# Performance work log

Measured on AMD Instinct MI355X. Metric: run time of the kernel, lower is better.

Reference implementation:

```python
import jax, jax.numpy as jnp
import numpy as np

D_MODEL = 1024
N_HEADS = 16
D_K = D_MODEL // N_HEADS
SCALE = float(np.sqrt(D_K))


def setup_inputs() -> dict:
    key = jax.random.key(0)
    ks = jax.random.split(key, 12)
    B, S = 2, 2048
    std = 1.0 / np.sqrt(D_MODEL)
    inp = {
        "query": jax.random.normal(ks[0], (B, S, D_MODEL), jnp.float32),
        "key": jax.random.normal(ks[1], (B, S, D_MODEL), jnp.float32),
        "value": jax.random.normal(ks[2], (B, S, D_MODEL), jnp.float32),
        "mask": jnp.ones((B, S), jnp.int32),
        "Wq": jax.random.normal(ks[3], (D_MODEL, D_MODEL), jnp.float32) * std,
        "bq": jnp.zeros((D_MODEL,), jnp.float32),
        "Wk": jax.random.normal(ks[4], (D_MODEL, D_MODEL), jnp.float32) * std,
        "bk": jnp.zeros((D_MODEL,), jnp.float32),
        "Wv": jax.random.normal(ks[5], (D_MODEL, D_MODEL), jnp.float32) * std,
        "bv": jnp.zeros((D_MODEL,), jnp.float32),
        "Wo": jax.random.normal(ks[6], (D_MODEL, D_MODEL), jnp.float32) * std,
        "bo": jnp.zeros((D_MODEL,), jnp.float32),
    }
    return inp


def reference(query, key, value, mask, Wq, bq, Wk, bk, Wv, bv, Wo, bo):
    B, S, _ = query.shape
    # projections -> [B, H, S, d_k]
    def proj(x, W, b):
        return (x @ W.T + b).reshape(B, S, N_HEADS, D_K).transpose(0, 2, 1, 3)

    Q = proj(query, Wq, bq)
    K = proj(key, Wk, bk)
    V = proj(value, Wv, bv)
    # [B, H, Sq, Sk] scores
    scores = jnp.einsum("bhqd,bhkd->bhqk", Q, K) / SCALE
    m = mask[:, None, None, :]  # broadcast over heads and query positions
    scores = jnp.where(m == 0, jnp.float32(-1e9), scores)
    attn = jax.nn.softmax(scores, axis=-1)
    # dropout is identity in eval mode
    context = jnp.einsum("bhqk,bhkd->bhqd", attn, V)
    context = context.transpose(0, 2, 1, 3).reshape(B, S, D_MODEL)
    return context @ Wo.T + bo
```

## Files before the change

kernel.cpp:

```cpp
#include <hip/hip_runtime.h>
#include <stdint.h>

#define D_MODEL 1024
#define NH 16
#define DK 64
#define BATCH 2
#define SEQ 2048
#define MROWS (BATCH*SEQ)

typedef float f32x4 __attribute__((ext_vector_type(4)));
typedef float f32x16 __attribute__((ext_vector_type(16)));
typedef __bf16 bf16x8 __attribute__((ext_vector_type(8)));

#define AS1 __attribute__((address_space(1)))
#define AS3 __attribute__((address_space(3)))

#if __has_builtin(__builtin_amdgcn_exp2f)
#define EXP2F(x) __builtin_amdgcn_exp2f(x)
#else
#define EXP2F(x) exp2f(x)
#endif
#if __has_builtin(__builtin_amdgcn_rcpf)
#define RCPF(x) __builtin_amdgcn_rcpf(x)
#else
#define RCPF(x) (1.0f/(x))
#endif

#define PERMSWAP(a, b) \
    asm volatile("s_nop 1\n\tv_permlane32_swap_b32 %0, %1" \
                 : "+v"(a), "+v"(b))

static __device__ __forceinline__ void gld_lds16(const void* g, void* l) {
    __builtin_amdgcn_global_load_lds((const AS1 unsigned int*)g,
                                     (AS3 unsigned int*)l, 16, 0, 0);
}

static __device__ __forceinline__ unsigned short bfbits(float f) {
    return __builtin_bit_cast(unsigned short, (__bf16)f);
}
static __device__ __forceinline__ unsigned int pk2bf(float a, float b) {
    return (unsigned int)bfbits(a) | ((unsigned int)bfbits(b) << 16);
}

static __device__ __forceinline__ float vmax16(const f32x16& v) {
    float a = fmaxf(fmaxf(v[0], v[1]), fmaxf(v[2], v[3]));
    float b = fmaxf(fmaxf(v[4], v[5]), fmaxf(v[6], v[7]));
    float c = fmaxf(fmaxf(v[8], v[9]), fmaxf(v[10], v[11]));
    float d = fmaxf(fmaxf(v[12], v[13]), fmaxf(v[14], v[15]));
    return fmaxf(fmaxf(a, b), fmaxf(c, d));
}

struct PrepArgs {
    const float* src[7];
    unsigned short* dst[7];
    int n4[7];
};

__global__ __launch_bounds__(256) void prep_cvt(PrepArgs a) {
    const int z = blockIdx.y;
    const float4* s = (const float4*)a.src[z];
    uint2* d = (uint2*)a.dst[z];
    const int n = a.n4[z];
    for (int i = blockIdx.x * blockDim.x + threadIdx.x; i < n;
         i += gridDim.x * blockDim.x) {
        float4 v = s[i];
        uint2 o;
        o.x = pk2bf(v.x, v.y);
        o.y = pk2bf(v.z, v.w);
        d[i] = o;
    }
}

struct GemmArgs {
    const unsigned short* A[3];
    const unsigned short* W[3];
    const float* bias[3];
    void* C[3];
    float scale[3];
    int hm[3];
};

template<bool OUT_F32, int BM, int BN>
__global__ __launch_bounds__(256) void gemm_bt(GemmArgs g) {
    constexpr int IM = BM / 32;
    constexpr int JN = BN / 32;
    __shared__ unsigned short As[BM * 64];
    __shared__ unsigned short Bs[BN * 64];
    const int z = blockIdx.z;
    const char* A = (const char*)g.A[z];
    const char* W = (const char*)g.W[z];
    const float* bias = g.bias[z];
    const float scale = g.scale[z];
    const int hm = g.hm[z];
    const int t = threadIdx.x;
    const int w = t >> 6, lane = t & 63;
    const int m0 = blockIdx.x * BM, n0 = blockIdx.y * BN;
    const int wm = (w >> 1) * (BM / 2), wn = (w & 1) * (BN / 2);

    const int srow = t >> 3;
    const int csw = ((t & 7) * 16) ^ ((srow & 7) << 4);
    const char* pA = A + (size_t)(m0 + srow) * 2048 + csw;
    const char* pW = W + (size_t)(n0 + srow) * 2048 + csw;

    f32x4 acc[IM][JN];
#pragma unroll
    for (int i = 0; i < IM; ++i)
#pragma unroll
        for (int j = 0; j < JN; ++j)
            acc[i][j] = (f32x4){0.f, 0.f, 0.f, 0.f};

    const int g4 = lane >> 4;
    const int kg16 = g4 * 16;
    const int swl = (lane & 7) << 4;

    for (int kt = 0; kt < 16; ++kt) {
        __syncthreads();
#pragma unroll
        for (int p = 0; p < IM; ++p)
            gld_lds16(pA + (size_t)p * (32 * 2048), &As[w * 512 + p * 2048]);
#pragma unroll
        for (int p = 0; p < JN; ++p)
            gld_lds16(pW + (size_t)p * (32 * 2048), &Bs[w * 512 + p * 2048]);
        pA += 128; pW += 128;
        __syncthreads();
#pragma unroll
        for (int ks = 0; ks < 2; ++ks) {
            bf16x8 af[IM], bfv[JN];
#pragma unroll
            for (int i = 0; i < IM; ++i) {
                int ra = wm + i * 16 + (lane & 15);
                af[i] = *(const bf16x8*)((const char*)As + ra * 128 +
                                         ((ks * 64 + kg16) ^ swl));
            }
#pragma unroll
            for (int j = 0; j < JN; ++j) {
                int rb = wn + j * 16 + (lane & 15);
                bfv[j] = *(const bf16x8*)((const char*)Bs + rb * 128 +
                                          ((ks * 64 + kg16) ^ swl));
            }
            __builtin_amdgcn_s_setprio(1);
#pragma unroll
            for (int i = 0; i < IM; ++i)
#pragma unroll
                for (int j = 0; j < JN; ++j)
                    acc[i][j] = __builtin_amdgcn_mfma_f32_16x16x32_bf16(
                        af[i], bfv[j], acc[i][j], 0, 0, 0);
            __builtin_amdgcn_s_setprio(0);
        }
    }

    float bj[JN];
#pragma unroll
    for (int j = 0; j < JN; ++j) bj[j] = bias[n0 + wn + j * 16 + (lane & 15)];

    if (hm == 2) {
#pragma unroll
        for (int i = 0; i < IM; ++i) {
            int row0 = m0 + wm + i * 16 + (g4 << 2);
            int bb = row0 >> 11, ss0 = row0 & 2047;
#pragma unroll
            for (int j = 0; j < JN; ++j) {
                int col = n0 + wn + j * 16 + (lane & 15);
                int hh = col >> 6, dd = col & 63;
                ushort4 o;
                o.x = bfbits(acc[i][j][0] + bj[j]);
                o.y = bfbits(acc[i][j][1] + bj[j]);
                o.z = bfbits(acc[i][j][2] + bj[j]);
                o.w = bfbits(acc[i][j][3] + bj[j]);
                *(ushort4*)((unsigned short*)g.C[z] +
                            (((size_t)(bb * 16 + hh) * 64 + dd) * 2048 + ss0)) = o;
            }
        }
        return;
    }

#pragma unroll
    for (int i = 0; i < IM; ++i)
#pragma unroll
        for (int r = 0; r < 4; ++r) {
            int row = m0 + wm + i * 16 + g4 * 4 + r;
#pragma unroll
            for (int j = 0; j < JN; ++j) {
                int col = n0 + wn + j * 16 + (lane & 15);
                float v = (acc[i][j][r] + bj[j]) * scale;
                if (OUT_F32) {
                    ((float*)g.C[z])[(size_t)row * 1024 + col] = v;
                } else if (hm) {
                    int bb = row >> 11, ss = row & 2047;
                    int hh = col >> 6, dd = col & 63;
                    ((unsigned short*)g.C[z])
                        [(((size_t)(bb * 16 + hh) * 2048) + ss) * 64 + dd] =
                        bfbits(v);
                } else {
                    ((unsigned short*)g.C[z])[(size_t)row * 1024 + col] =
                        bfbits(v);
                }
            }
        }
}

__global__ __launch_bounds__(256) void attn_fwd(
    const unsigned short* __restrict__ Qh,
    const unsigned short* __restrict__ Kh,
    const unsigned short* __restrict__ VtT,
    const int* __restrict__ mask,
    unsigned short* __restrict__ Ctx) {
    __shared__ unsigned short KlA[4096], KlB[4096];
    __shared__ unsigned short VlA[4096], VlB[4096];
    __shared__ int cfl[4];

    const int wg = blockIdx.x + (int)gridDim.x * blockIdx.y;
    const int swzid = (wg & 7) * 64 + (wg >> 3);
    const int qt = swzid & 15, bh = swzid >> 4;
    const int b = bh >> 4, h = bh & 15;

    const int t = threadIdx.x, w = t >> 6, lane = t & 63;
    const int hi = lane >> 5, q5 = lane & 31;
    const int swl5 = (q5 & 7) << 4;

    const int* mbase = mask + b * SEQ;
    int myclean = 1;
#pragma unroll
    for (int i = 0; i < 2; ++i) {
        int4 m4 = ((const int4*)mbase)[t + i * 256];
        myclean &= (m4.x != 0) & (m4.y != 0) & (m4.z != 0) & (m4.w != 0);
    }
    int wc = __all(myclean);
    if (lane == 0) cfl[w] = wc;

    const char* Qbase = (const char*)Qh + (size_t)bh * 2048 * 128;
    const int qrow = qt * 128 + w * 32 + q5;
    bf16x8 qf[4];
#pragma unroll
    for (int t4 = 0; t4 < 4; ++t4)
        qf[t4] = *(const bf16x8*)(Qbase + (size_t)qrow * 128 +
                                  t4 * 32 + hi * 16);

    f32x16 cacc[2];
#pragma unroll
    for (int r = 0; r < 16; ++r) { cacc[0][r] = 0.f; cacc[1][r] = 0.f; }
    float mstate = -3e38f, lstate = 0.f;

    const char* Kbyte = (const char*)Kh + (size_t)bh * 2048 * 128;
    const char* Vbyte = (const char*)VtT + (size_t)bh * 64 * 4096;

    const int srow = t >> 3;
    const int csw = ((t & 7) * 16) ^ ((srow & 7) << 4);
    const size_t srow128 = (size_t)srow * 128;
    const size_t srow4096 = (size_t)srow * 4096;

    auto stage = [&](unsigned short* Kd, unsigned short* Vd, int kv0) {
        const char* ks = Kbyte + (size_t)kv0 * 128;
        gld_lds16(ks + srow128 + csw,               Kd + w * 512);
        gld_lds16(ks + srow128 + 32 * 128 + csw,    Kd + 2048 + w * 512);
        const char* vs = Vbyte + (size_t)kv0 * 2;
        gld_lds16(vs + srow4096 + csw,              Vd + w * 512);
        gld_lds16(vs + srow4096 + 32 * 4096 + csw,  Vd + 2048 + w * 512);
    };

    __syncthreads();
    const int clean = cfl[0] & cfl[1] & cfl[2] & cfl[3];

    auto compute = [&](const unsigned short* Kl, const unsigned short* Vl,
                       int kv0) {
        f32x16 sacc[2];
#pragma unroll
        for (int r = 0; r < 16; ++r) { sacc[0][r] = 0.f; sacc[1][r] = 0.f; }
#pragma unroll
        for (int t4 = 0; t4 < 4; ++t4) {
            int off = (t4 * 32 + hi * 16) ^ swl5;
            bf16x8 kf0 = *(const bf16x8*)((const char*)Kl + q5 * 128 + off);
            bf16x8 kf1 = *(const bf16x8*)((const char*)Kl + (32 + q5) * 128 + off);
            __builtin_amdgcn_s_setprio(1);
            sacc[0] = __builtin_amdgcn_mfma_f32_32x32x16_bf16(
                kf0, qf[t4], sacc[0], 0, 0, 0);
            sacc[1] = __builtin_amdgcn_mfma_f32_32x32x16_bf16(
                kf1, qf[t4], sacc[1], 0, 0, 0);
            __builtin_amdgcn_s_setprio(0);
        }

        if (!clean) {
#pragma unroll
            for (int kb = 0; kb < 2; ++kb)
#pragma unroll
                for (int r = 0; r < 16; ++r) {
                    int key = kb * 32 + (r & 3) + 8 * (r >> 2) + 4 * hi;
                    if (mbase[kv0 + key] == 0) sacc[kb][r] = -1e9f;
                }
        }

        float vm = fmaxf(vmax16(sacc[0]), vmax16(sacc[1]));
        vm = fmaxf(vm, __shfl_xor(vm, 32));

        if (!__all(vm <= mstate + 8.f)) {
            float mnew = fmaxf(mstate, vm);
            float sc = EXP2F(mstate - mnew);
            mstate = mnew;
            lstate *= sc;
#pragma unroll
            for (int r = 0; r < 16; ++r) {
                float scb = __shfl(sc, (r & 3) + 8 * (r >> 2) + 4 * hi);
                cacc[0][r] *= scb;
                cacc[1][r] *= scb;
            }
        }

        const float mn = mstate;
        float ssum = 0.f;
        unsigned int Ap[2][4], Bp[2][4];
#pragma unroll
        for (int kb = 0; kb < 2; ++kb)
#pragma unroll
            for (int si = 0; si < 4; ++si) {
                float e0 = EXP2F(sacc[kb][4 * si + 0] - mn);
                float e1 = EXP2F(sacc[kb][4 * si + 1] - mn);
                float e2 = EXP2F(sacc[kb][4 * si + 2] - mn);
                float e3 = EXP2F(sacc[kb][4 * si + 3] - mn);
                ssum += (e0 + e1) + (e2 + e3);
                Ap[kb][si] = pk2bf(e0, e1);
                Bp[kb][si] = pk2bf(e2, e3);
            }
        ssum += __shfl_xor(ssum, 32);
        lstate += ssum;

#pragma unroll
        for (int ct = 0; ct < 4; ++ct) {
            const int kb = ct >> 1, sA = (ct & 1) * 2;
            unsigned int w0 = Ap[kb][sA], w2 = Ap[kb][sA + 1];
            unsigned int w1 = Bp[kb][sA], w3 = Bp[kb][sA + 1];
            PERMSWAP(w0, w2);
            PERMSWAP(w1, w3);
            union { unsigned int u[4]; bf16x8 v; } pa;
            pa.u[0] = w0; pa.u[1] = w1; pa.u[2] = w2; pa.u[3] = w3;

            int off = (ct * 32 + hi * 16) ^ swl5;
            bf16x8 vf0 = *(const bf16x8*)((const char*)Vl + q5 * 128 + off);
            bf16x8 vf1 = *(const bf16x8*)((const char*)Vl + (32 + q5) * 128 + off);
            __builtin_amdgcn_s_setprio(1);
            cacc[0] = __builtin_amdgcn_mfma_f32_32x32x16_bf16(
                pa.v, vf0, cacc[0], 0, 0, 0);
            cacc[1] = __builtin_amdgcn_mfma_f32_32x32x16_bf16(
                pa.v, vf1, cacc[1], 0, 0, 0);
            __builtin_amdgcn_s_setprio(0);
        }
    };

    stage(KlA, VlA, 0);
    __syncthreads();
    for (int i = 0; i < 16; ++i) {
        const int kv0 = i * 128;
        if (kv0 + 64 < SEQ) stage(KlB, VlB, kv0 + 64);
        compute(KlA, VlA, kv0);
        __syncthreads();
        if (kv0 + 128 < SEQ) stage(KlA, VlA, kv0 + 128);
        compute(KlB, VlB, kv0 + 64);
        __syncthreads();
    }

    const float inv = RCPF(lstate);
#pragma unroll
    for (int r = 0; r < 16; ++r) {
        int cr = (r & 3) + 8 * (r >> 2) + 4 * hi;
        float invr = __shfl(inv, cr);
        size_t row = (size_t)b * SEQ + qt * 128 + w * 32 + cr;
        Ctx[row * 1024 + h * 64 + q5]      = bfbits(cacc[0][r] * invr);
        Ctx[row * 1024 + h * 64 + 32 + q5] = bfbits(cacc[1][r] * invr);
    }
}

extern "C" void kernel_launch(void* const* d_in, const int* in_sizes, int n_in,
                              void* d_out, int out_size, void* d_ws, size_t ws_size,
                              hipStream_t stream) {
    const float* q   = (const float*)d_in[0];
    const float* k   = (const float*)d_in[1];
    const float* v   = (const float*)d_in[2];
    const int* mask  = (const int*)d_in[3];
    const float* Wq  = (const float*)d_in[4];
    const float* bq  = (const float*)d_in[5];
    const float* Wk  = (const float*)d_in[6];
    const float* bk  = (const float*)d_in[7];
    const float* Wv  = (const float*)d_in[8];
    const float* bv  = (const float*)d_in[9];
    const float* Wo  = (const float*)d_in[10];
    const float* bo  = (const float*)d_in[11];

    unsigned short* ws = (unsigned short*)d_ws;
    const size_t NX = (size_t)MROWS * D_MODEL;
    const size_t NW = (size_t)D_MODEL * D_MODEL;
    unsigned short* Xq  = ws;
    unsigned short* Xk  = Xq + NX;
    unsigned short* Xv  = Xk + NX;
    unsigned short* Wqb = Xv + NX;
    unsigned short* Wkb = Wqb + NW;
    unsigned short* Wvb = Wkb + NW;
    unsigned short* Wob = Wvb + NW;
    unsigned short* Qhd = Wob + NW;
    unsigned short* Khd = Qhd + NX;
    unsigned short* Vtt = Khd + NX;
    unsigned short* Cx  = Vtt + NX;

    PrepArgs pa;
    pa.src[0] = q;  pa.src[1] = k;  pa.src[2] = v;
    pa.src[3] = Wq; pa.src[4] = Wk; pa.src[5] = Wv; pa.src[6] = Wo;
    pa.dst[0] = Xq;  pa.dst[1] = Xk;  pa.dst[2] = Xv;
    pa.dst[3] = Wqb; pa.dst[4] = Wkb; pa.dst[5] = Wvb; pa.dst[6] = Wob;
    for (int i = 0; i < 3; ++i) pa.n4[i] = (int)(NX / 4);
    for (int i = 3; i < 7; ++i) pa.n4[i] = (int)(NW / 4);
    prep_cvt<<<dim3(256, 7), dim3(256), 0, stream>>>(pa);

    GemmArgs gq;
    gq.A[0] = Xq;  gq.A[1] = Xk;  gq.A[2] = Xv;
    gq.W[0] = Wqb; gq.W[1] = Wkb; gq.W[2] = Wvb;
    gq.bias[0] = bq; gq.bias[1] = bk; gq.bias[2] = bv;
    gq.C[0] = Qhd; gq.C[1] = Khd; gq.C[2] = Vtt;
    gq.scale[0] = 0.125f * 1.44269504088896340736f;
    gq.scale[1] = 1.f; gq.scale[2] = 1.f;
    gq.hm[0] = 1; gq.hm[1] = 1; gq.hm[2] = 2;
    gemm_bt<false, 128, 128><<<dim3(32, 8, 3), dim3(256), 0, stream>>>(gq);

    attn_fwd<<<dim3(16, 32), dim3(256), 0, stream>>>(Qhd, Khd, Vtt, mask, Cx);

    GemmArgs go;
    go.A[0] = Cx; go.W[0] = Wob; go.bias[0] = bo; go.C[0] = d_out;
    go.scale[0] = 1.f; go.hm[0] = 0;
    go.A[1] = go.A[2] = nullptr; go.W[1] = go.W[2] = nullptr;
    go.bias[1] = go.bias[2] = nullptr; go.C[1] = go.C[2] = nullptr;
    go.scale[1] = go.scale[2] = 1.f; go.hm[1] = go.hm[2] = 0;
    gemm_bt<true, 128, 64><<<dim3(32, 16, 1), dim3(256), 0, stream>>>(go);
}
```

Baseline: 234.5 us.

## Split attention KV range in two with a separate softmax-combine kernel

Splits each attention workgroup's 2048-key sweep into two halves run by separate workgroups, doubling the grid from 512 to 1024 blocks. Each half writes unnormalized bf16 partial outputs plus running max and sum to reused workspace buffers. A new combine kernel merges them with log-sum-exp weights before the output projection. The aim is better CU occupancy on the many-CU GPU, at the cost of extra partial-result traffic, an extra launch, and an additional bf16 rounding of partials.

```diff
diff --git a/kernel.cpp b/kernel.cpp
--- a/kernel.cpp
+++ b/kernel.cpp
@@ -40,6 +40,9 @@
 }
 static __device__ __forceinline__ unsigned int pk2bf(float a, float b) {
     return (unsigned int)bfbits(a) | ((unsigned int)bfbits(b) << 16);
+}
+static __device__ __forceinline__ float bf2f(unsigned int u) {
+    return __builtin_bit_cast(float, u << 16);
 }
 
 static __device__ __forceinline__ float vmax16(const f32x16& v) {
@@ -204,27 +207,27 @@
     const unsigned short* __restrict__ Kh,
     const unsigned short* __restrict__ VtT,
     const int* __restrict__ mask,
-    unsigned short* __restrict__ Ctx) {
+    unsigned short* __restrict__ Opart,
+    float* __restrict__ Mlf,
+    float* __restrict__ Llf) {
     __shared__ unsigned short KlA[4096], KlB[4096];
     __shared__ unsigned short VlA[4096], VlB[4096];
     __shared__ int cfl[4];
 
-    const int wg = blockIdx.x + (int)gridDim.x * blockIdx.y;
-    const int swzid = (wg & 7) * 64 + (wg >> 3);
-    const int qt = swzid & 15, bh = swzid >> 4;
+    const int wg = blockIdx.x + (int)gridDim.x *
+                   (blockIdx.y + (int)gridDim.y * blockIdx.z);
+    const int swz = (wg & 7) * 128 + (wg >> 3);
+    const int sp = swz & 1, qt = (swz >> 1) & 15, bh = swz >> 5;
     const int b = bh >> 4, h = bh & 15;
+    const int kvb = sp * 1024;
 
     const int t = threadIdx.x, w = t >> 6, lane = t & 63;
     const int hi = lane >> 5, q5 = lane & 31;
     const int swl5 = (q5 & 7) << 4;
 
     const int* mbase = mask + b * SEQ;
-    int myclean = 1;
-#pragma unroll
-    for (int i = 0; i < 2; ++i) {
-        int4 m4 = ((const int4*)mbase)[t + i * 256];
-        myclean &= (m4.x != 0) & (m4.y != 0) & (m4.z != 0) & (m4.w != 0);
-    }
+    int4 m4 = ((const int4*)(mbase + kvb))[t];
+    int myclean = (m4.x != 0) & (m4.y != 0) & (m4.z != 0) & (m4.w != 0);
     int wc = __all(myclean);
     if (lane == 0) cfl[w] = wc;
 
@@ -345,27 +348,62 @@
         }
     };
 
-    stage(KlA, VlA, 0);
+    stage(KlA, VlA, kvb);
     __syncthreads();
-    for (int i = 0; i < 16; ++i) {
-        const int kv0 = i * 128;
-        if (kv0 + 64 < SEQ) stage(KlB, VlB, kv0 + 64);
+    for (int i = 0; i < 8; ++i) {
+        const int kv0 = kvb + i * 128;
+        stage(KlB, VlB, kv0 + 64);
         compute(KlA, VlA, kv0);
         __syncthreads();
-        if (kv0 + 128 < SEQ) stage(KlA, VlA, kv0 + 128);
+        if (i < 7) stage(KlA, VlA, kv0 + 128);
         compute(KlB, VlB, kv0 + 64);
         __syncthreads();
     }
 
-    const float inv = RCPF(lstate);
 #pragma unroll
     for (int r = 0; r < 16; ++r) {
         int cr = (r & 3) + 8 * (r >> 2) + 4 * hi;
-        float invr = __shfl(inv, cr);
-        size_t row = (size_t)b * SEQ + qt * 128 + w * 32 + cr;
-        Ctx[row * 1024 + h * 64 + q5]      = bfbits(cacc[0][r] * invr);
-        Ctx[row * 1024 + h * 64 + 32 + q5] = bfbits(cacc[1][r] * invr);
-    }
+        size_t row = (size_t)(sp * 4096 + b * 2048 + qt * 128 + w * 32 + cr);
+        Opart[row * 1024 + h * 64 + q5]      = bfbits(cacc[0][r]);
+        Opart[row * 1024 + h * 64 + 32 + q5] = bfbits(cacc[1][r]);
+    }
+    if (hi == 0) {
+        const int li = sp * 65536 + bh * 2048 + qt * 128 + w * 32 + q5;
+        Mlf[li] = mstate;
+        Llf[li] = lstate;
+    }
+}
+
+__global__ __launch_bounds__(256) void attn_combine(
+    const unsigned short* __restrict__ Op,
+    const float* __restrict__ Mlf,
+    const float* __restrict__ Llf,
+    unsigned short* __restrict__ Cx) {
+    const int idx = blockIdx.x * 256 + threadIdx.x;
+    const int row = idx >> 7;
+    const int c8 = (idx & 127) << 3;
+    const int b = row >> 11, s = row & 2047, h = c8 >> 6;
+    const int li = (b * 16 + h) * 2048 + s;
+    const float m1 = Mlf[li], m2 = Mlf[65536 + li];
+    const float l1 = Llf[li], l2 = Llf[65536 + li];
+    const float mx = fmaxf(m1, m2);
+    float w1 = EXP2F(m1 - mx), w2 = EXP2F(m2 - mx);
+    const float inv = RCPF(fmaf(l1, w1, l2 * w2));
+    w1 *= inv; w2 *= inv;
+    const uint4 o1 = *(const uint4*)(Op + (size_t)row * 1024 + c8);
+    const uint4 o2 = *(const uint4*)(Op + (size_t)(4096 + row) * 1024 + c8);
+    uint4 o;
+    unsigned int rr[4];
+#pragma unroll
+    for (int j = 0; j < 4; ++j) {
+        unsigned int a = ((const unsigned int*)&o1)[j];
+        unsigned int c = ((const unsigned int*)&o2)[j];
+        float x0 = bf2f(a & 0xffffu) * w1 + bf2f(c & 0xffffu) * w2;
+        float x1 = bf2f(a >> 16) * w1 + bf2f(c >> 16) * w2;
+        rr[j] = pk2bf(x0, x1);
+    }
+    o.x = rr[0]; o.y = rr[1]; o.z = rr[2]; o.w = rr[3];
+    *(uint4*)(Cx + (size_t)row * 1024 + c8) = o;
 }
 
 extern "C" void kernel_launch(void* const* d_in, const int* in_sizes, int n_in,
@@ -418,7 +456,13 @@
     gq.hm[0] = 1; gq.hm[1] = 1; gq.hm[2] = 2;
     gemm_bt<false, 128, 128><<<dim3(32, 8, 3), dim3(256), 0, stream>>>(gq);
 
-    attn_fwd<<<dim3(16, 32), dim3(256), 0, stream>>>(Qhd, Khd, Vtt, mask, Cx);
+    unsigned short* Opart = Xq;
+    float* Mlf = (float*)Xv;
+    float* Llf = Mlf + 2 * 65536;
+    attn_fwd<<<dim3(16, 32, 2), dim3(256), 0, stream>>>(
+        Qhd, Khd, Vtt, mask, Opart, Mlf, Llf);
+
+    attn_combine<<<dim3(2048), dim3(256), 0, stream>>>(Opart, Mlf, Llf, Cx);
 
     GemmArgs go;
     go.A[0] = Cx; go.W[0] = Wob; go.bias[0] = bo; go.C[0] = d_out;
```

New measurement: 241.1 us. 2.8% more time.
